# Kernel tuning notes

Hardware: AMD Instinct MI355X
Metric: run time of the kernel (lower is better)

The kernel has to match this reference:

```python
import jax, jax.numpy as jnp
import numpy as np

H = 128
R = 14
B = 2048
TYPES = ['operator', 'table', 'column', 'predicate', 'operation', 'literal', 'numeral']
SIZES = {'operator': 100000, 'table': 20000, 'column': 120000, 'predicate': 60000,
         'operation': 100000, 'literal': 50000, 'numeral': 50000}
FEAT = {'operator': 4, 'table': 2, 'column': 10, 'predicate': 4, 'operation': 8,
        'literal': 1, 'numeral': 1}
# (name, src_type, dst_type, num_edges), order matches edge_type_mapping in the torch module
EDGES = [('ei_scannedby', 'table', 'operator', 100000),
         ('ei_pred_filters', 'predicate', 'operator', 100000),
         ('ei_outputby', 'column', 'operator', 100000),
         ('ei_col_connects', 'column', 'operation', 100000),
         ('ei_calledby', 'operator', 'operator', 100000),
         ('ei_op_filters', 'operation', 'operator', 100000),
         ('ei_op_connects', 'operation', 'predicate', 100000),
         ('ei_lit_connects', 'literal', 'operation', 100000),
         ('ei_num_connects', 'numeral', 'operation', 100000),
         ('ei_lit_self', 'literal', 'literal', 50000),
         ('ei_num_self', 'numeral', 'numeral', 50000),
         ('ei_tab_self', 'table', 'table', 20000),
         ('ei_col_self', 'column', 'column', 120000),
         ('ei_pred_self', 'predicate', 'predicate', 60000)]
OFFS = {}
_o = 0
for _t in TYPES:
    OFFS[_t] = _o
    _o += SIZES[_t]
N_TOTAL = _o


def setup_inputs():
    key = jax.random.key(0)
    ks = iter(jax.random.split(key, 64))
    inp = {}
    for t in TYPES:
        inp['x_' + t] = jax.random.normal(next(ks), (SIZES[t], FEAT[t]), jnp.float32)
    for name, s, d, E in EDGES:
        src = jax.random.randint(next(ks), (E,), 0, SIZES[s], jnp.int32)
        dst = jax.random.randint(next(ks), (E,), 0, SIZES[d], jnp.int32)
        inp[name] = jnp.stack([src, dst])
    inp['batch_operator'] = jnp.sort(
        jax.random.randint(next(ks), (SIZES['operator'],), 0, B, jnp.int32))

    def lin_w(k, din, dout):
        s = 1.0 / float(np.sqrt(din))
        return jax.random.uniform(k, (din, dout), jnp.float32, -s, s)

    for t in TYPES:
        inp['W_' + t] = lin_w(next(ks), FEAT[t], H)
        inp['b_' + t] = jnp.zeros((H,), jnp.float32)
    for c in ('c1', 'c2'):
        inp[c + '_root'] = lin_w(next(ks), H, H)
        inp[c + '_rel'] = jax.random.normal(next(ks), (R, H, H), jnp.float32) / float(np.sqrt(H))
        inp[c + '_bias'] = jnp.zeros((H,), jnp.float32)
    inp['n1_g'] = jnp.ones((H,), jnp.float32); inp['n1_b'] = jnp.zeros((H,), jnp.float32)
    inp['n2_g'] = jnp.ones((H,), jnp.float32); inp['n2_b'] = jnp.zeros((H,), jnp.float32)
    inp['W_lin'] = lin_w(next(ks), H, 1)
    inp['b_lin'] = jnp.zeros((1,), jnp.float32)
    return inp


def layer_norm(x, g, b, eps=1e-5):
    mu = jnp.mean(x, axis=-1, keepdims=True)
    var = jnp.var(x, axis=-1, keepdims=True)
    return (x - mu) * jax.lax.rsqrt(var + eps) * g + b


def rgcn(x, rel_edges, w_root, w_rel, bias):
    # PyG RGCNConv: root transform + per-relation gather -> GEMM -> scatter-mean into dst
    out = x @ w_root
    for r, (src, dst) in enumerate(rel_edges):
        msg = x[src] @ w_rel[r]  # [E_r, H]
        agg = jax.ops.segment_sum(msg, dst, num_segments=N_TOTAL)
        cnt = jax.ops.segment_sum(jnp.ones(src.shape, x.dtype), dst, num_segments=N_TOTAL)
        out = out + agg / jnp.maximum(cnt, 1.0)[:, None]
    return out + bias


def reference(x_operator, x_table, x_column, x_predicate, x_operation, x_literal, x_numeral,
              ei_scannedby, ei_pred_filters, ei_outputby, ei_col_connects, ei_calledby,
              ei_op_filters, ei_op_connects, ei_lit_connects, ei_num_connects, ei_lit_self,
              ei_num_self, ei_tab_self, ei_col_self, ei_pred_self, batch_operator,
              W_operator, b_operator, W_table, b_table, W_column, b_column,
              W_predicate, b_predicate, W_operation, b_operation, W_literal, b_literal,
              W_numeral, b_numeral, c1_root, c1_rel, c1_bias, c2_root, c2_rel, c2_bias,
              n1_g, n1_b, n2_g, n2_b, W_lin, b_lin):
    # per-node-type input embedding, then concat in fixed type order
    x = jnp.concatenate([
        x_operator @ W_operator + b_operator,
        x_table @ W_table + b_table,
        x_column @ W_column + b_column,
        x_predicate @ W_predicate + b_predicate,
        x_operation @ W_operation + b_operation,
        x_literal @ W_literal + b_literal,
        x_numeral @ W_numeral + b_numeral], axis=0)
    eis = [ei_scannedby, ei_pred_filters, ei_outputby, ei_col_connects, ei_calledby,
           ei_op_filters, ei_op_connects, ei_lit_connects, ei_num_connects, ei_lit_self,
           ei_num_self, ei_tab_self, ei_col_self, ei_pred_self]
    rel_edges = [(e[0] + OFFS[s], e[1] + OFFS[d]) for e, (_, s, d, _) in zip(eis, EDGES)]
    h = rgcn(x, rel_edges, c1_root, c1_rel, c1_bias)
    h = layer_norm(jax.nn.elu(h), n1_g, n1_b)  # dropout is identity in eval mode
    h = rgcn(h, rel_edges, c2_root, c2_rel, c2_bias)
    h = layer_norm(jax.nn.elu(h), n2_g, n2_b)
    op = h[:SIZES['operator']]  # operator offset is 0
    cnt = jax.ops.segment_sum(jnp.ones((op.shape[0],), op.dtype), batch_operator, num_segments=B)
    pooled = jax.ops.segment_sum(op, batch_operator, num_segments=B) / jnp.maximum(cnt, 1.0)[:, None]
    return (pooled @ W_lin + b_lin)[:, 0]  # [B]
```

## Files before the change

kernel.cpp:

```cpp
#include <hip/hip_runtime.h>
#include <hip/hip_bf16.h>
#include <math.h>

#define HD 128
#define N_OP 100000
#define N_L1 400000
#define NB 2048
#define CNT_TOT 1160000
#define EDG_TOT 1100000

typedef short short8 __attribute__((ext_vector_type(8)));
typedef float floatx4 __attribute__((ext_vector_type(4)));

static const int REL_E[14]    = {100000,100000,100000,100000,100000,100000,100000,100000,100000,50000,50000,20000,120000,60000};
static const int REL_DSZ[14]  = {100000,100000,100000,100000,100000,100000,60000,100000,100000,50000,50000,20000,120000,60000};
static const int CNT_OFF[14]  = {0,100000,200000,300000,400000,500000,600000,660000,760000,860000,910000,960000,980000,1100000};
static const int SRC_T[14] = {1,3,2,2,0,4,4,5,6,5,6,1,2,3};
static const int TF[7]  = {4,2,10,4,8,1,1};
static const size_t AGR_OFF[14] = {0,200000,600000,1600000,2600000,3000000,3800000,4280000,4380000,0,0,4480000,4520000,5720000};
#define AGR_TOT 5960000
static const int RELW[14] = {4,7,12,93,23,28,70,104,106,-1,-1,40,54,79};
static const int RELI[14] = {6,11,22,103,27,36,78,105,107,-1,-1,42,64,83};
static const int ROOTW[5] = {0,38,44,66,85};
static const int ROOTB[5] = {37,43,65,84,108};
#define WL1_ROWS 109

__device__ inline unsigned short f2bf(float f) {
  union { float f; unsigned int u; } v; v.f = f;
  unsigned int r = v.u + 0x7FFF + ((v.u >> 16) & 1);
  return (unsigned short)(r >> 16);
}
__device__ inline float bfu2f(unsigned short u) {
  union { unsigned int i; float f; } v; v.i = ((unsigned int)u) << 16; return v.f;
}

struct CJob { const int* dst; int coff; int E; int blk0; };
struct CPackK { CJob j[12]; int bblk0; const int* batch; float* pcnt; int nop; };

__global__ void count_k(CPackK P, int* __restrict__ ICNT) {
  int b = blockIdx.x;
  if (b >= P.bblk0) {
    int i = (b - P.bblk0) * 256 + threadIdx.x;
    if (i < P.nop) atomicAdd(&P.pcnt[P.batch[i]], 1.0f);
    return;
  }
  int ji = 0;
#pragma unroll
  for (int i = 1; i < 12; ++i) if (b >= P.j[i].blk0) ji = i;
  CJob J = P.j[ji];
  int e = (b - J.blk0) * 256 + threadIdx.x;
  if (e < J.E) atomicAdd(&ICNT[J.coff + J.dst[e]], 1);
}

#define SCAN_BLK 1024
__global__ void scan1(const int* __restrict__ in, int* __restrict__ out,
                      int* __restrict__ bsum, int n) {
  __shared__ int sh[256];
  int t = threadIdx.x;
  int base = blockIdx.x * SCAN_BLK + t * 4;
  int v0 = 0, v1 = 0, v2 = 0, v3 = 0;
  if (base + 3 < n) { int4 q = *(const int4*)&in[base]; v0 = q.x; v1 = q.y; v2 = q.z; v3 = q.w; }
  else {
    if (base < n) v0 = in[base];
    if (base + 1 < n) v1 = in[base + 1];
    if (base + 2 < n) v2 = in[base + 2];
    if (base + 3 < n) v3 = in[base + 3];
  }
  int ts = v0 + v1 + v2 + v3;
  sh[t] = ts; __syncthreads();
  for (int o = 1; o < 256; o <<= 1) {
    int x = (t >= o) ? sh[t - o] : 0;
    __syncthreads();
    sh[t] += x;
    __syncthreads();
  }
  int excl = sh[t] - ts;
  if (base < n) out[base] = excl;
  if (base + 1 < n) out[base + 1] = excl + v0;
  if (base + 2 < n) out[base + 2] = excl + v0 + v1;
  if (base + 3 < n) out[base + 3] = excl + v0 + v1 + v2;
  if (t == 255) bsum[blockIdx.x] = sh[255];
}

__global__ void scan2(int* __restrict__ bs, int nb) {
  __shared__ int sh[256];
  int t = threadIdx.x;
  const int C = 5;
  int v[C]; int ts = 0;
#pragma unroll
  for (int i = 0; i < C; ++i) { int idx = t * C + i; v[i] = (idx < nb) ? bs[idx] : 0; ts += v[i]; }
  sh[t] = ts; __syncthreads();
  for (int o = 1; o < 256; o <<= 1) {
    int x = (t >= o) ? sh[t - o] : 0;
    __syncthreads();
    sh[t] += x;
    __syncthreads();
  }
  int run = sh[t] - ts;
#pragma unroll
  for (int i = 0; i < C; ++i) { int idx = t * C + i; if (idx < nb) bs[idx] = run; run += v[i]; }
}

__global__ void scan3(int* __restrict__ CUR, int2* __restrict__ OFF2,
                      const int* __restrict__ ICNT, const int* __restrict__ bs, int n) {
  int i = blockIdx.x * 256 + threadIdx.x;
  if (i < n) {
    int o = CUR[i] + bs[i >> 10];
    CUR[i] = o;
    OFF2[i] = make_int2(o, ICNT[i]);
  }
}

struct FJob { const int* src; const int* dst; int coff; int E; int blk0; };
struct FPackK { FJob j[12]; };

__global__ void fill_k(FPackK P, int* __restrict__ CUR, int* __restrict__ EDG) {
  int b = blockIdx.x;
  int ji = 0;
#pragma unroll
  for (int i = 1; i < 12; ++i) if (b >= P.j[i].blk0) ji = i;
  FJob J = P.j[ji];
  int e = (b - J.blk0) * 256 + threadIdx.x;
  if (e < J.E) {
    int pos = atomicAdd(&CUR[J.coff + J.dst[e]], 1);
    EDG[pos] = J.src[e];
  }
}

struct GJob { const float* x; float* agr; int coff; int D; int F; int blk0; };
struct GPack { GJob j[12]; };

template <int F>
__device__ inline void gathF(const float* __restrict__ x, float* __restrict__ agr,
                             const int* __restrict__ EDG, int2 oc, int d) {
  if (oc.y == 0) return;
  float s[F];
#pragma unroll
  for (int f = 0; f < F; ++f) s[f] = 0.f;
  for (int e = 0; e < oc.y; ++e) {
    int si = EDG[oc.x + e];
    const float* xp = &x[(size_t)si * F];
#pragma unroll
    for (int f = 0; f < F; ++f) s[f] += xp[f];
  }
  float rc = 1.0f / (float)oc.y;
  float* ap = &agr[(size_t)d * F];
#pragma unroll
  for (int f = 0; f < F; ++f) ap[f] = s[f] * rc;
}

__global__ void gather_all(GPack P, const int2* __restrict__ OFF2, const int* __restrict__ EDG) {
  int b = blockIdx.x;
  int ji = 0;
#pragma unroll
  for (int i = 1; i < 12; ++i) if (b >= P.j[i].blk0) ji = i;
  GJob J = P.j[ji];
  int d = (b - J.blk0) * 256 + threadIdx.x;
  if (d >= J.D) return;
  int2 oc = OFF2[J.coff + d];
  switch (J.F) {
    case 1:  gathF<1>(J.x, J.agr, EDG, oc, d); break;
    case 2:  gathF<2>(J.x, J.agr, EDG, oc, d); break;
    case 4:  gathF<4>(J.x, J.agr, EDG, oc, d); break;
    case 8:  gathF<8>(J.x, J.agr, EDG, oc, d); break;
    default: gathF<10>(J.x, J.agr, EDG, oc, d); break;
  }
}

struct CombJob { const float* A; const float* bin; const float* Mtx; const float* extra; float* Wout; float* bout; int F; };
struct CombPack { CombJob j[17]; };

__global__ void weights_prep(CombPack P, const float* __restrict__ c2root,
                             const float* __restrict__ c2rel, __hip_bfloat16* __restrict__ Wt) {
  int b = blockIdx.x;
  if (b < 17) {
    if (threadIdx.x >= 128) return;
    CombJob J = P.j[b];
    int c = threadIdx.x;
    for (int f = 0; f <= J.F; ++f) {
      const float* arow = (f < J.F) ? &J.A[f * HD] : J.bin;
      float s = (f < J.F) ? 0.f : (J.extra ? J.extra[c] : 0.f);
      for (int k = 0; k < HD; ++k) s = fmaf(arow[k], J.Mtx[k * HD + c], s);
      if (f < J.F) J.Wout[f * HD + c] = s;
      else J.bout[c] = s;
    }
  } else {
    const int RID[6] = {-1, 0, 1, 2, 4, 5};
    int j = b - 17;
    const float* W = (j == 0) ? c2root : (c2rel + (size_t)RID[j] * HD * HD);
    __hip_bfloat16* o = Wt + (size_t)j * 16384;
    for (int i = threadIdx.x; i < 16384; i += 256) {
      int i8 = i & 7;
      int ln = (i >> 3) & 63;
      int k4 = (i >> 9) & 3;
      int nt = i >> 11;
      int ln15 = ln & 15, quad = ln >> 4;
      int k = k4 * 32 + quad * 8 + i8;
      int n = nt * 16 + ln15;
      o[i] = __float2bfloat16(W[k * 128 + n]);
    }
  }
}

struct L1v2 {
  const float* x0; const float* x1; const float* x2; const float* x3; const float* x4;
  const float* AGR; const float* WL1; const int2* OFF2;
  const float* g; const float* b;
  unsigned short* Hb;
};

__device__ inline void ldv2(float* s, const float* __restrict__ p) {
  float2 v = *(const float2*)p; s[0] = v.x; s[1] = v.y;
}
__device__ inline void ldv4(float* s, const float* __restrict__ p) {
  float4 v = *(const float4*)p; s[0] = v.x; s[1] = v.y; s[2] = v.z; s[3] = v.w;
}
__device__ inline void relF1(float* s, const float* __restrict__ agr,
                             const int2* __restrict__ OFF2, int cb, int row) {
  if (OFF2[cb + row].y > 0) { s[0] = agr[row]; s[1] = 1.f; }
  else { s[0] = 0.f; s[1] = 0.f; }
}
__device__ inline void relF2(float* s, const float* __restrict__ agr,
                             const int2* __restrict__ OFF2, int cb, int row) {
  if (OFF2[cb + row].y > 0) { ldv2(s, &agr[(size_t)row * 2]); s[2] = 1.f; }
  else { s[0] = s[1] = s[2] = 0.f; }
}
__device__ inline void relF4(float* s, const float* __restrict__ agr,
                             const int2* __restrict__ OFF2, int cb, int row) {
  if (OFF2[cb + row].y > 0) { ldv4(s, &agr[(size_t)row * 4]); s[4] = 1.f; }
  else {
#pragma unroll
    for (int f = 0; f < 5; ++f) s[f] = 0.f;
  }
}
__device__ inline void relF8(float* s, const float* __restrict__ agr,
                             const int2* __restrict__ OFF2, int cb, int row) {
  if (OFF2[cb + row].y > 0) {
    ldv4(s, &agr[(size_t)row * 8]); ldv4(s + 4, &agr[(size_t)row * 8 + 4]); s[8] = 1.f;
  } else {
#pragma unroll
    for (int f = 0; f < 9; ++f) s[f] = 0.f;
  }
}
__device__ inline void relF10(float* s, const float* __restrict__ agr,
                              const int2* __restrict__ OFF2, int cb, int row) {
  if (OFF2[cb + row].y > 0) {
    const float* p = &agr[(size_t)row * 10];
#pragma unroll
    for (int j = 0; j < 5; ++j) ldv2(s + 2 * j, p + 2 * j);
    s[10] = 1.f;
  } else {
#pragma unroll
    for (int f = 0; f < 11; ++f) s[f] = 0.f;
  }
}

template <int KT>
__device__ inline void l1_dot8(const float* __restrict__ Ls, const float (&s)[KT],
                               int c4, float (&a)[8]) {
  {
    float4 w0 = *(const float4*)&Ls[KT * 128 + c4];
    float4 w1 = *(const float4*)&Ls[KT * 128 + c4 + 64];
    a[0] = w0.x; a[1] = w0.y; a[2] = w0.z; a[3] = w0.w;
    a[4] = w1.x; a[5] = w1.y; a[6] = w1.z; a[7] = w1.w;
  }
#pragma unroll
  for (int k = 0; k < KT; ++k) {
    float4 w0 = *(const float4*)&Ls[k * 128 + c4];
    float4 w1 = *(const float4*)&Ls[k * 128 + c4 + 64];
    a[0] = fmaf(s[k], w0.x, a[0]); a[1] = fmaf(s[k], w0.y, a[1]);
    a[2] = fmaf(s[k], w0.z, a[2]); a[3] = fmaf(s[k], w0.w, a[3]);
    a[4] = fmaf(s[k], w1.x, a[4]); a[5] = fmaf(s[k], w1.y, a[5]);
    a[6] = fmaf(s[k], w1.z, a[6]); a[7] = fmaf(s[k], w1.w, a[7]);
  }
}

__device__ inline void l1_fin8(float (&a)[8], int c4, const float* __restrict__ g,
                               const float* __restrict__ bb,
                               unsigned short* __restrict__ Hb, int orow) {
  float p = 0.f, q = 0.f;
#pragma unroll
  for (int j = 0; j < 8; ++j) {
    a[j] = (a[j] > 0.f) ? a[j] : (expf(a[j]) - 1.f);
    p += a[j]; q += a[j] * a[j];
  }
#pragma unroll
  for (int m = 8; m >= 1; m >>= 1) {
    p += __shfl_xor(p, m, 64);
    q += __shfl_xor(q, m, 64);
  }
  float mean = p * (1.0f / HD);
  float var = q * (1.0f / HD) - mean * mean;
  float rstd = rsqrtf(var + 1e-5f);
  float4 g0 = *(const float4*)&g[c4], g1 = *(const float4*)&g[c4 + 64];
  float4 b0 = *(const float4*)&bb[c4], b1 = *(const float4*)&bb[c4 + 64];
  float gg[8] = {g0.x, g0.y, g0.z, g0.w, g1.x, g1.y, g1.z, g1.w};
  float bv[8] = {b0.x, b0.y, b0.z, b0.w, b1.x, b1.y, b1.z, b1.w};
  float o[8];
#pragma unroll
  for (int j = 0; j < 8; ++j) o[j] = (a[j] - mean) * rstd * gg[j] + bv[j];
  uint2 lo, hi;
  lo.x = (unsigned int)f2bf(o[0]) | ((unsigned int)f2bf(o[1]) << 16);
  lo.y = (unsigned int)f2bf(o[2]) | ((unsigned int)f2bf(o[3]) << 16);
  hi.x = (unsigned int)f2bf(o[4]) | ((unsigned int)f2bf(o[5]) << 16);
  hi.y = (unsigned int)f2bf(o[6]) | ((unsigned int)f2bf(o[7]) << 16);
  *(uint2*)&Hb[(size_t)orow * HD + c4] = lo;
  *(uint2*)&Hb[(size_t)orow * HD + c4 + 64] = hi;
}

__global__ __launch_bounds__(256) void layer1_v5(L1v2 A) {
  __shared__ float Ls[38 * 128];
  const int b = blockIdx.x, t = threadIdx.x;
  const int wv = t >> 6, ln = t & 63;
  const int sub = ln >> 4, c4 = (ln & 15) * 4;
  int type, seg;
  if (b < 1563) { type = 0; seg = b; }
  else if (b < 1876) { type = 1; seg = b - 1563; }
  else if (b < 3751) { type = 2; seg = b - 1876; }
  else if (b < 4689) { type = 3; seg = b - 3751; }
  else { type = 4; seg = b - 4689; }
  const int NR[5] = {38, 6, 22, 19, 24};
  const int RB[5] = {0, 38, 44, 66, 85};
  const int TR[5] = {100000, 20000, 120000, 60000, 100000};
  const int OB[5] = {0, 100000, 120000, 240000, 300000};
  {
    const float4* src = (const float4*)(A.WL1 + RB[type] * 128);
    float4* dst = (float4*)Ls;
    int n4 = NR[type] * 32;
    for (int i = t; i < n4; i += 256) dst[i] = src[i];
  }
  __syncthreads();
  const int row0 = seg * 64, M = TR[type], ob = OB[type];

  if (type == 0) {
#pragma unroll
    for (int it = 0; it < 4; ++it) {
      int row = row0 + it * 16 + wv * 4 + sub;
      if (row >= M) continue;
      float s[37];
      ldv4(s, &A.x0[(size_t)row * 4]);
      relF2(s + 4, A.AGR + 0, A.OFF2, 0, row);
      relF4(s + 7, A.AGR + 200000, A.OFF2, 100000, row);
      relF10(s + 12, A.AGR + 600000, A.OFF2, 200000, row);
      relF4(s + 23, A.AGR + 2600000, A.OFF2, 400000, row);
      relF8(s + 28, A.AGR + 3000000, A.OFF2, 500000, row);
      float a[8];
      l1_dot8<37>(Ls, s, c4, a);
      l1_fin8(a, c4, A.g, A.b, A.Hb, ob + row);
    }
  } else if (type == 1) {
#pragma unroll
    for (int it = 0; it < 4; ++it) {
      int row = row0 + it * 16 + wv * 4 + sub;
      if (row >= M) continue;
      float s[5];
      ldv2(s, &A.x1[(size_t)row * 2]);
      relF2(s + 2, A.AGR + 4480000, A.OFF2, 960000, row);
      float a[8];
      l1_dot8<5>(Ls, s, c4, a);
      l1_fin8(a, c4, A.g, A.b, A.Hb, ob + row);
    }
  } else if (type == 2) {
#pragma unroll
    for (int it = 0; it < 4; ++it) {
      int row = row0 + it * 16 + wv * 4 + sub;
      if (row >= M) continue;
      float s[21];
      const float* p = &A.x2[(size_t)row * 10];
#pragma unroll
      for (int j = 0; j < 5; ++j) ldv2(s + 2 * j, p + 2 * j);
      relF10(s + 10, A.AGR + 4520000, A.OFF2, 980000, row);
      float a[8];
      l1_dot8<21>(Ls, s, c4, a);
      l1_fin8(a, c4, A.g, A.b, A.Hb, ob + row);
    }
  } else if (type == 3) {
#pragma unroll
    for (int it = 0; it < 4; ++it) {
      int row = row0 + it * 16 + wv * 4 + sub;
      if (row >= M) continue;
      float s[18];
      ldv4(s, &A.x3[(size_t)row * 4]);
      relF8(s + 4, A.AGR + 3800000, A.OFF2, 600000, row);
      relF4(s + 13, A.AGR + 5720000, A.OFF2, 1100000, row);
      float a[8];
      l1_dot8<18>(Ls, s, c4, a);
      l1_fin8(a, c4, A.g, A.b, A.Hb, ob + row);
    }
  } else {
#pragma unroll
    for (int it = 0; it < 4; ++it) {
      int row = row0 + it * 16 + wv * 4 + sub;
      if (row >= M) continue;
      float s[23];
      ldv4(s, &A.x4[(size_t)row * 8]);
      ldv4(s + 4, &A.x4[(size_t)row * 8 + 4]);
      relF10(s + 8, A.AGR + 1600000, A.OFF2, 300000, row);
      relF1(s + 19, A.AGR + 4280000, A.OFF2, 660000, row);
      relF1(s + 21, A.AGR + 4380000, A.OFF2, 760000, row);
      float a[8];
      l1_dot8<23>(Ls, s, c4, a);
      l1_fin8(a, c4, A.g, A.b, A.Hb, ob + row);
    }
  }
}

__global__ __launch_bounds__(256, 4)
void l2_fused(const unsigned short* __restrict__ Hb, const unsigned short* __restrict__ Wt,
              const int2* __restrict__ OFF2, const int* __restrict__ EDG,
              const float* __restrict__ c2bias, const float* __restrict__ n2g,
              const float* __restrict__ n2b, const float* __restrict__ Wl,
              const int* __restrict__ batch, float* __restrict__ accb, int M) {
  const int CSR_OFF[5] = {0, 100000, 200000, 400000, 500000};
  const int SOFF[5]    = {100000, 240000, 120000, 0, 300000};
  const int t = threadIdx.x, wv = t >> 6, ln = t & 63;
  const int quad = ln >> 4, ln15 = ln & 15, q8 = quad * 8;
  const int m0 = blockIdx.x * 64;
  const int rowA = m0 + wv * 16 + ln15;

  int2 ocs[5];
#pragma unroll
  for (int r = 0; r < 5; ++r)
    ocs[r] = (rowA < M) ? OFF2[CSR_OFF[r] + rowA] : make_int2(0, 0);

  float bias_c[8], gw[8];
  float pg = 0.f, pb = 0.f;
#pragma unroll
  for (int nt = 0; nt < 8; ++nt) {
    int col = nt * 16 + ln15;
    float wl = Wl[col], gc = n2g[col], bc = n2b[col];
    bias_c[nt] = c2bias[col];
    gw[nt] = gc * wl;
    pg += gc * wl;
    pb += bc * wl;
  }
#pragma unroll
  for (int m = 8; m >= 1; m >>= 1) {
    pg += __shfl_xor(pg, m, 64);
    pb += __shfl_xor(pb, m, 64);
  }

  floatx4 acc[8];
#pragma unroll
  for (int b = 0; b < 8; ++b) acc[b] = (floatx4){0.f, 0.f, 0.f, 0.f};

  for (int term = 0; term < 6; ++term) {
    short8 afr[4];
    if (term == 0) {
      if (rowA < M) {
#pragma unroll
        for (int k4 = 0; k4 < 4; ++k4)
          afr[k4] = *(const short8*)&Hb[(size_t)rowA * HD + k4 * 32 + q8];
      } else {
#pragma unroll
        for (int k4 = 0; k4 < 4; ++k4)
#pragma unroll
          for (int j = 0; j < 8; ++j) afr[k4][j] = 0;
      }
    } else {
      float sum[4][8];
#pragma unroll
      for (int k4 = 0; k4 < 4; ++k4)
#pragma unroll
        for (int j = 0; j < 8; ++j) sum[k4][j] = 0.f;
      int2 oc = ocs[term - 1];
      if (oc.y > 0) {
        int so = SOFF[term - 1];
        for (int e = 0; e < oc.y; ++e) {
          size_t s = (size_t)(EDG[oc.x + e] + so);
#pragma unroll
          for (int k4 = 0; k4 < 4; ++k4) {
            short8 h = *(const short8*)&Hb[s * HD + k4 * 32 + q8];
#pragma unroll
            for (int j = 0; j < 8; ++j) sum[k4][j] += bfu2f((unsigned short)h[j]);
          }
        }
        float rc = 1.0f / (float)oc.y;
#pragma unroll
        for (int k4 = 0; k4 < 4; ++k4)
#pragma unroll
          for (int j = 0; j < 8; ++j) sum[k4][j] *= rc;
      }
#pragma unroll
      for (int k4 = 0; k4 < 4; ++k4)
#pragma unroll
        for (int j = 0; j < 8; ++j) afr[k4][j] = (short)f2bf(sum[k4][j]);
    }

    const unsigned short* wb = Wt + (size_t)term * 16384 + (size_t)ln * 8;
#pragma unroll
    for (int nt = 0; nt < 8; ++nt) {
      short8 b0 = *(const short8*)(wb + nt * 2048 + 0 * 512);
      short8 b1 = *(const short8*)(wb + nt * 2048 + 1 * 512);
      short8 b2 = *(const short8*)(wb + nt * 2048 + 2 * 512);
      short8 b3 = *(const short8*)(wb + nt * 2048 + 3 * 512);
      acc[nt] = __builtin_amdgcn_mfma_f32_16x16x32_bf16(afr[0], b0, acc[nt], 0, 0, 0);
      acc[nt] = __builtin_amdgcn_mfma_f32_16x16x32_bf16(afr[1], b1, acc[nt], 0, 0, 0);
      acc[nt] = __builtin_amdgcn_mfma_f32_16x16x32_bf16(afr[2], b2, acc[nt], 0, 0, 0);
      acc[nt] = __builtin_amdgcn_mfma_f32_16x16x32_bf16(afr[3], b3, acc[nt], 0, 0, 0);
    }
  }

#pragma unroll
  for (int r = 0; r < 4; ++r) {
    int rowD = m0 + wv * 16 + quad * 4 + r;
    float p = 0.f, q = 0.f, s1 = 0.f;
#pragma unroll
    for (int nt = 0; nt < 8; ++nt) {
      float v = acc[nt][r] + bias_c[nt];
      float e = (v > 0.f) ? v : (expf(v) - 1.f);
      p += e; q += e * e; s1 += e * gw[nt];
    }
#pragma unroll
    for (int m = 8; m >= 1; m >>= 1) {
      p += __shfl_xor(p, m, 64);
      q += __shfl_xor(q, m, 64);
      s1 += __shfl_xor(s1, m, 64);
    }
    if (ln15 == 0 && rowD < M) {
      float mean = p * (1.0f / HD);
      float var = q * (1.0f / HD) - mean * mean;
      float rstd = rsqrtf(var + 1e-5f);
      float o = rstd * (s1 - mean * pg) + pb;
      atomicAdd(&accb[batch[rowD]], o);
    }
  }
}

__global__ void final_kernel(const float* __restrict__ accb, const float* __restrict__ pcnt,
                             const float* __restrict__ bl, float* __restrict__ out) {
  int b = blockIdx.x * 256 + threadIdx.x;
  if (b < NB) out[b] = accb[b] / fmaxf(pcnt[b], 1.0f) + bl[0];
}

extern "C" void kernel_launch(void* const* d_in, const int* in_sizes, int n_in,
                              void* d_out, int out_size, void* d_ws, size_t ws_size,
                              hipStream_t stream) {
  const float* xt[7];
  for (int t = 0; t < 7; ++t) xt[t] = (const float*)d_in[t];
  const int* ei[14];
  for (int r = 0; r < 14; ++r) ei[r] = (const int*)d_in[7 + r];
  const int* batch = (const int*)d_in[21];
  const float* Wemb[7]; const float* bemb[7];
  for (int t = 0; t < 7; ++t) { Wemb[t] = (const float*)d_in[22 + 2 * t]; bemb[t] = (const float*)d_in[23 + 2 * t]; }
  const float* c_root[2] = {(const float*)d_in[36], (const float*)d_in[39]};
  const float* c_rel[2]  = {(const float*)d_in[37], (const float*)d_in[40]};
  const float* c_bias[2] = {(const float*)d_in[38], (const float*)d_in[41]};
  const float* ng[2] = {(const float*)d_in[42], (const float*)d_in[44]};
  const float* nbv[2] = {(const float*)d_in[43], (const float*)d_in[45]};
  const float* Wlin = (const float*)d_in[46];
  const float* blin = (const float*)d_in[47];
  float* out = (float*)d_out;

  char* base = (char*)d_ws;
  size_t off = 0;
  auto alloc = [&](size_t bytes) -> void* {
    void* p = base + off;
    off += (bytes + 255) & ~(size_t)255;
    return p;
  };
  __hip_bfloat16* Hb = (__hip_bfloat16*)alloc((size_t)N_L1 * HD * 2);
  float* AGR  = (float*)alloc((size_t)AGR_TOT * 4);
  int*   ICNT = (int*)alloc((size_t)CNT_TOT * 4);
  int*   CUR  = (int*)alloc((size_t)CNT_TOT * 4);
  int2*  OFF2 = (int2*)alloc((size_t)CNT_TOT * 8);
  int*   EDG  = (int*)alloc((size_t)EDG_TOT * 4);
  int*   BS   = (int*)alloc((size_t)1152 * 4);
  float* WL1  = (float*)alloc((size_t)WL1_ROWS * 128 * 4);
  __hip_bfloat16* WT3 = (__hip_bfloat16*)alloc((size_t)6 * 16384 * 2);
  float* ACC  = (float*)alloc((size_t)NB * 4);
  float* PCNT = (float*)alloc((size_t)NB * 4);

  static const int l1_rels[12] = {0,1,2,3,4,5,6,7,8,11,12,13};

  hipMemsetAsync(ICNT, 0, (size_t)CNT_TOT * 4, stream);
  hipMemsetAsync(ACC, 0, (size_t)2 * NB * 4, stream);

  CPackK CP1;
  int blk = 0;
  for (int q = 0; q < 12; ++q) {
    int r = l1_rels[q];
    CP1.j[q].dst = ei[r] + REL_E[r];
    CP1.j[q].coff = CNT_OFF[r];
    CP1.j[q].E = REL_E[r];
    CP1.j[q].blk0 = blk;
    blk += (REL_E[r] + 255) / 256;
  }
  CP1.bblk0 = blk; CP1.batch = batch; CP1.pcnt = PCNT; CP1.nop = N_OP;
  blk += (N_OP + 255) / 256;
  count_k<<<blk, 256, 0, stream>>>(CP1, ICNT);

  int nb1 = (CNT_TOT + SCAN_BLK - 1) / SCAN_BLK;
  scan1<<<nb1, 256, 0, stream>>>(ICNT, CUR, BS, CNT_TOT);
  scan2<<<1, 256, 0, stream>>>(BS, nb1);
  scan3<<<(CNT_TOT + 255) / 256, 256, 0, stream>>>(CUR, OFF2, ICNT, BS, CNT_TOT);

  FPackK FP;
  blk = 0;
  for (int q = 0; q < 12; ++q) {
    int r = l1_rels[q];
    FP.j[q].src = ei[r];
    FP.j[q].dst = ei[r] + REL_E[r];
    FP.j[q].coff = CNT_OFF[r];
    FP.j[q].E = REL_E[r];
    FP.j[q].blk0 = blk;
    blk += (REL_E[r] + 255) / 256;
  }
  fill_k<<<blk, 256, 0, stream>>>(FP, CUR, EDG);

  CombPack CP;
  for (int q = 0; q < 12; ++q) {
    int r = l1_rels[q]; int t = SRC_T[r];
    CombJob& J = CP.j[q];
    J.A = Wemb[t]; J.bin = bemb[t]; J.Mtx = c_rel[0] + (size_t)r * HD * HD;
    J.extra = nullptr;
    J.Wout = WL1 + (size_t)RELW[r] * 128;
    J.bout = WL1 + (size_t)RELI[r] * 128;
    J.F = TF[t];
  }
  for (int t = 0; t < 5; ++t) {
    CombJob& J = CP.j[12 + t];
    J.A = Wemb[t]; J.bin = bemb[t]; J.Mtx = c_root[0];
    J.extra = c_bias[0];
    J.Wout = WL1 + (size_t)ROOTW[t] * 128;
    J.bout = WL1 + (size_t)ROOTB[t] * 128;
    J.F = TF[t];
  }
  weights_prep<<<23, 256, 0, stream>>>(CP, c_root[1], c_rel[1], WT3);

  GPack GP;
  blk = 0;
  for (int q = 0; q < 12; ++q) {
    int r = l1_rels[q]; int t = SRC_T[r];
    GP.j[q].x = xt[t];
    GP.j[q].agr = AGR + AGR_OFF[r];
    GP.j[q].coff = CNT_OFF[r];
    GP.j[q].D = REL_DSZ[r];
    GP.j[q].F = TF[t];
    GP.j[q].blk0 = blk;
    blk += (REL_DSZ[r] + 255) / 256;
  }
  gather_all<<<blk, 256, 0, stream>>>(GP, OFF2, EDG);

  L1v2 A;
  A.x0 = xt[0]; A.x1 = xt[1]; A.x2 = xt[2]; A.x3 = xt[3]; A.x4 = xt[4];
  A.AGR = AGR; A.WL1 = WL1; A.OFF2 = OFF2;
  A.g = ng[0]; A.b = nbv[0]; A.Hb = (unsigned short*)Hb;
  layer1_v5<<<6252, 256, 0, stream>>>(A);

  l2_fused<<<(N_OP + 63) / 64, 256, 0, stream>>>(
      (const unsigned short*)Hb, (const unsigned short*)WT3,
      OFF2, EDG, c_bias[1], ng[1], nbv[1], Wlin, batch, ACC, N_OP);

  final_kernel<<<(NB + 255) / 256, 256, 0, stream>>>(ACC, PCNT, blin, out);
}
```

Before: 602.7 us.

## Split layer-2 relation terms across waves with shared-memory reduction

Each block of the fused layer-2 kernel now handles 16 rows instead of 64, and the six relation terms (root plus five gathered neighbour means) are split across the four waves, which get 2, 1, 1 and 2 terms. Partial MFMA accumulators are combined through shared-memory atomic adds before the ELU/LayerNorm/pooling epilogue, which is now spread over all 256 threads. The aim is to cut the serial per-wave gather chain and balance the irregular neighbour loads, at the cost of four times as many blocks, extra LDS atomics and two barriers per block.

```diff
diff --git a/kernel.cpp b/kernel.cpp
--- a/kernel.cpp
+++ b/kernel.cpp
@@ -413,40 +413,28 @@
               const int* __restrict__ batch, float* __restrict__ accb, int M) {
   const int CSR_OFF[5] = {0, 100000, 200000, 400000, 500000};
   const int SOFF[5]    = {100000, 240000, 120000, 0, 300000};
+  __shared__ float Csh[16 * 132];
   const int t = threadIdx.x, wv = t >> 6, ln = t & 63;
   const int quad = ln >> 4, ln15 = ln & 15, q8 = quad * 8;
-  const int m0 = blockIdx.x * 64;
-  const int rowA = m0 + wv * 16 + ln15;
-
-  int2 ocs[5];
-#pragma unroll
-  for (int r = 0; r < 5; ++r)
-    ocs[r] = (rowA < M) ? OFF2[CSR_OFF[r] + rowA] : make_int2(0, 0);
-
-  float bias_c[8], gw[8];
-  float pg = 0.f, pb = 0.f;
-#pragma unroll
-  for (int nt = 0; nt < 8; ++nt) {
-    int col = nt * 16 + ln15;
-    float wl = Wl[col], gc = n2g[col], bc = n2b[col];
-    bias_c[nt] = c2bias[col];
-    gw[nt] = gc * wl;
-    pg += gc * wl;
-    pb += bc * wl;
-  }
-#pragma unroll
-  for (int m = 8; m >= 1; m >>= 1) {
-    pg += __shfl_xor(pg, m, 64);
-    pb += __shfl_xor(pb, m, 64);
-  }
+  const int m0 = blockIdx.x * 16;
+  const int rowA = m0 + ln15;
+
+  for (int i = t; i < 16 * 132; i += 256) Csh[i] = 0.f;
+
+  int tl0, tl1, ntm;
+  if (wv == 0)      { tl0 = -1; tl1 = 0; ntm = 2; }
+  else if (wv == 1) { tl0 = 1;  tl1 = 0; ntm = 1; }
+  else if (wv == 2) { tl0 = 2;  tl1 = 0; ntm = 1; }
+  else              { tl0 = 3;  tl1 = 4; ntm = 2; }
 
   floatx4 acc[8];
 #pragma unroll
   for (int b = 0; b < 8; ++b) acc[b] = (floatx4){0.f, 0.f, 0.f, 0.f};
 
-  for (int term = 0; term < 6; ++term) {
+  for (int q = 0; q < ntm; ++q) {
+    int tl = (q == 0) ? tl0 : tl1;
     short8 afr[4];
-    if (term == 0) {
+    if (tl < 0) {
       if (rowA < M) {
 #pragma unroll
         for (int k4 = 0; k4 < 4; ++k4)
@@ -463,9 +451,9 @@
       for (int k4 = 0; k4 < 4; ++k4)
 #pragma unroll
         for (int j = 0; j < 8; ++j) sum[k4][j] = 0.f;
-      int2 oc = ocs[term - 1];
+      int2 oc = (rowA < M) ? OFF2[CSR_OFF[tl] + rowA] : make_int2(0, 0);
       if (oc.y > 0) {
-        int so = SOFF[term - 1];
+        int so = SOFF[tl];
         for (int e = 0; e < oc.y; ++e) {
           size_t s = (size_t)(EDG[oc.x + e] + so);
 #pragma unroll
@@ -487,7 +475,7 @@
         for (int j = 0; j < 8; ++j) afr[k4][j] = (short)f2bf(sum[k4][j]);
     }
 
-    const unsigned short* wb = Wt + (size_t)term * 16384 + (size_t)ln * 8;
+    const unsigned short* wb = Wt + (size_t)(tl + 1) * 16384 + (size_t)ln * 8;
 #pragma unroll
     for (int nt = 0; nt < 8; ++nt) {
       short8 b0 = *(const short8*)(wb + nt * 2048 + 0 * 512);
@@ -501,23 +489,43 @@
     }
   }
 
-#pragma unroll
-  for (int r = 0; r < 4; ++r) {
-    int rowD = m0 + wv * 16 + quad * 4 + r;
-    float p = 0.f, q = 0.f, s1 = 0.f;
-#pragma unroll
-    for (int nt = 0; nt < 8; ++nt) {
-      float v = acc[nt][r] + bias_c[nt];
+  __syncthreads();
+#pragma unroll
+  for (int nt = 0; nt < 8; ++nt)
+#pragma unroll
+    for (int r = 0; r < 4; ++r)
+      atomicAdd(&Csh[(quad * 4 + r) * 132 + nt * 16 + ln15], acc[nt][r]);
+  __syncthreads();
+
+  {
+    int g = t >> 4, i15 = t & 15, cb = i15 * 8;
+    int rowD = m0 + g;
+    float4 wl0 = *(const float4*)&Wl[cb],    wl1 = *(const float4*)&Wl[cb + 4];
+    float4 gg0 = *(const float4*)&n2g[cb],   gg1 = *(const float4*)&n2g[cb + 4];
+    float4 nb0 = *(const float4*)&n2b[cb],   nb1 = *(const float4*)&n2b[cb + 4];
+    float4 bc0 = *(const float4*)&c2bias[cb], bc1 = *(const float4*)&c2bias[cb + 4];
+    float wlv[8] = {wl0.x, wl0.y, wl0.z, wl0.w, wl1.x, wl1.y, wl1.z, wl1.w};
+    float ggv[8] = {gg0.x, gg0.y, gg0.z, gg0.w, gg1.x, gg1.y, gg1.z, gg1.w};
+    float nbv[8] = {nb0.x, nb0.y, nb0.z, nb0.w, nb1.x, nb1.y, nb1.z, nb1.w};
+    float bcv[8] = {bc0.x, bc0.y, bc0.z, bc0.w, bc1.x, bc1.y, bc1.z, bc1.w};
+    float p = 0.f, q = 0.f, s1 = 0.f, pg = 0.f, pb = 0.f;
+#pragma unroll
+    for (int j = 0; j < 8; ++j) {
+      float v = Csh[g * 132 + cb + j] + bcv[j];
       float e = (v > 0.f) ? v : (expf(v) - 1.f);
-      p += e; q += e * e; s1 += e * gw[nt];
+      float gw = ggv[j] * wlv[j];
+      p += e; q += e * e; s1 += e * gw;
+      pg += gw; pb += nbv[j] * wlv[j];
     }
 #pragma unroll
     for (int m = 8; m >= 1; m >>= 1) {
       p += __shfl_xor(p, m, 64);
       q += __shfl_xor(q, m, 64);
       s1 += __shfl_xor(s1, m, 64);
-    }
-    if (ln15 == 0 && rowD < M) {
+      pg += __shfl_xor(pg, m, 64);
+      pb += __shfl_xor(pb, m, 64);
+    }
+    if (i15 == 0 && rowD < M) {
       float mean = p * (1.0f / HD);
       float var = q * (1.0f / HD) - mean * mean;
       float rstd = rsqrtf(var + 1e-5f);
@@ -648,7 +656,7 @@
   A.g = ng[0]; A.b = nbv[0]; A.Hb = (unsigned short*)Hb;
   layer1_v5<<<6252, 256, 0, stream>>>(A);
 
-  l2_fused<<<(N_OP + 63) / 64, 256, 0, stream>>>(
+  l2_fused<<<(N_OP + 15) / 16, 256, 0, stream>>>(
       (const unsigned short*)Hb, (const unsigned short*)WT3,
       OFF2, EDG, c_bias[1], ng[1], nbv[1], Wlin, batch, ACC, N_OP);
 
```

New measurement: 877.4 us. 1.46x slower.
